# Kernel tuning notes

Hardware: AMD Instinct MI355X
Metric: run time of the kernel (lower is better)

The kernel has to match this reference:

```python
import jax, jax.numpy as jnp
import numpy as np

# Problem dims (match init_kwargs)
N, D, H, W = 32, 64, 56, 56      # Xshape
F, P = 128, 4                    # n_filters, number_of_points
KH = 3                           # h_filter == w_filter
PAD = KH // 2                    # padw
ALPHA = 0.1                      # threshold sharpness for sigmoid approximation


def setup_inputs() -> dict:
    key = jax.random.key(0)
    k1, k2, k3 = jax.random.split(key, 3)
    return {
        "input": jax.random.normal(k1, (N, D, H, W), dtype=jnp.float32),
        # integer kernel coordinates in [0, KH): (filter, point, [ky, kx])
        "kernels": jax.random.randint(k2, (F, P, 2), 0, KH, dtype=jnp.int32),
        # channel projection indices in [0, D): (filter, point)
        "projection_map": jax.random.randint(k3, (F, P), 0, D, dtype=jnp.int32),
    }


def _lbp_forward(x, kernels, projection_map):
    # Pad spatially by PAD (zero padding), as the CUDA kernel pads input.
    xp = jnp.pad(x, ((0, 0), (0, 0), (PAD, PAD), (PAD, PAD)))  # [N, D, H+2P, W+2P]

    # Per (filter, point): gather the HxW window at integer offset (ky, kx)
    # from channel c of the padded input. vmap of dynamic_slice -> one fused gather.
    def sample(c, ky, kx):
        return jax.lax.dynamic_slice(xp, (0, c, ky, kx), (N, 1, H, W))[:, 0]  # [N,H,W]

    samp = jax.vmap(jax.vmap(sample))(
        projection_map, kernels[..., 0], kernels[..., 1]
    )  # [F, P, N, H, W]
    samp = jnp.transpose(samp, (2, 0, 1, 3, 4))  # [N, F, P, H, W]

    # Center pixel (same channel as the sampled point).
    center = xp[:, :, PAD:PAD + H, PAD:PAD + W]       # [N, D, H, W]
    cen = center[:, projection_map]                    # [N, F, P, H, W]

    # Output0: per-point sampled difference; threshold approximated by a
    # steep sigmoid (scale 1/ALPHA) so the op is differentiable, then pool
    # the P bits into a binary code with weights 2^p.
    diff = samp - cen                                  # [N, F, P, H, W]
    bits = jax.nn.sigmoid(diff / ALPHA)
    weights = jnp.asarray(2.0 ** np.arange(P), dtype=jnp.float32)  # [P]
    return jnp.einsum('nfphw,p->nfhw', bits, weights)  # [N, F, H, W]


def reference(input, kernels, projection_map):
    return _lbp_forward(input, kernels, projection_map)
```

## Files before the change

### kernel.cpp

```cpp
#include <hip/hip_runtime.h>


#define NN 32
#define DD 64
#define HH 56
#define WW 56
#define FF 128
#define PP 4

#define ROWS 4
#define TR   (ROWS + 2)
#define TC   64
#define COL0 4
#define CHS  (TR * TC)
#define TILE_DW (DD * CHS)
#define NTHREADS 1024
#define NWAVES 16
#define NPAIR 16
#define NSTRIP (HH / ROWS)
#define FITER (FF / NWAVES)
#define ITEMS (DD * TR * 14)
#define NSLOT 6
#define IMGSTR (DD * HH * WW)

typedef _Float16 h2 __attribute__((ext_vector_type(2)));

static __device__ __forceinline__ uint32_t h2u(h2 h) {
    union { h2 h; uint32_t u; } v; v.h = h; return v.u;
}
static __device__ __forceinline__ h2 u2h(uint32_t u) {
    union { h2 h; uint32_t u; } v; v.u = u; return v.h;
}
static __device__ __forceinline__ h2 splat(float f) {
    h2 r; r.x = (_Float16)f; r.y = (_Float16)f; return r;
}
static __device__ __forceinline__ uint32_t pack2(float a, float b) {
    h2 r; r.x = (_Float16)a; r.y = (_Float16)b; return h2u(r);
}

__global__ __launch_bounds__(NTHREADS, 4) void lbp_kernel(
    const float* __restrict__ x,
    const int*   __restrict__ kern,
    const int*   __restrict__ proj,
    float*       __restrict__ out)
{
    __shared__ uint32_t tile[TILE_DW];

    const int tid = threadIdx.x;
    const int pr  = blockIdx.x;
    const int h0  = blockIdx.y * ROWS;

    const float* x0 = x + (size_t)pr * IMGSTR;
    const float* x1 = x0 + (size_t)NPAIR * IMGSTR;

    float4 av[NSLOT], bv[NSLOT];
    int    lo[NSLOT];
#pragma unroll
    for (int it = 0; it < NSLOT; ++it) {
        const int item = tid + it * NTHREADS;
        av[it] = make_float4(0.f, 0.f, 0.f, 0.f);
        bv[it] = make_float4(0.f, 0.f, 0.f, 0.f);
        lo[it] = -1;
        if (item < ITEMS) {
            const int ch  = item / (TR * 14);
            const int rem = item - ch * (TR * 14);
            const int tr  = rem / 14;
            const int v   = rem - tr * 14;
            lo[it] = ch * CHS + tr * TC + COL0 + 4 * v;
            const int h = h0 + tr - 1;
            if ((unsigned)h < (unsigned)HH) {
                const int off = ch * (HH * WW) + h * WW + 4 * v;
                av[it] = *(const float4*)(x0 + off);
                bv[it] = *(const float4*)(x1 + off);
            }
        }
    }

    if (tid < DD * TR * 2) {
        const int side = tid & 1;
        const int cr   = tid >> 1;
        tile[cr * TC + (side ? 60 : 3)] = 0u;
    }

#pragma unroll
    for (int it = 0; it < NSLOT; ++it) {
        if (lo[it] >= 0) {
            uint4 q;
            q.x = pack2(av[it].x, bv[it].x);
            q.y = pack2(av[it].y, bv[it].y);
            q.z = pack2(av[it].z, bv[it].z);
            q.w = pack2(av[it].w, bv[it].w);
            *(uint4*)(tile + lo[it]) = q;
        }
    }
    __syncthreads();

    const int wid  = __builtin_amdgcn_readfirstlane(tid >> 6);
    const int lane = tid & 63;
    const int w    = lane < WW ? lane : WW - 1;
    const bool act = lane < WW;
    const int cb   = TC + COL0 + w;

    const h2 K0a = splat(2.5f),     K0b = splat(-0.0078f);
    const h2 K1a = splat(1.49146f), K1b = splat(0.08455f);
    const h2 K2a = splat(0.45177f), K2b = splat(0.30774f);
    const h2 KF  = splat(0.49140f);
    const h2 INI = splat(7.5f);

    int f = wid;
    int4 pj = *(const int4*)(proj + f * PP);
    int4 ka = *(const int4*)(kern + f * (PP * 2));
    int4 kb = *(const int4*)(kern + f * (PP * 2) + 4);

#pragma unroll
    for (int k = 0; k < FITER; ++k) {
        const int fn = f + NWAVES;
        int4 pjn = pj, kan = ka, kbn = kb;
        if (k + 1 < FITER) {
            pjn = *(const int4*)(proj + fn * PP);
            kan = *(const int4*)(kern + fn * (PP * 2));
            kbn = *(const int4*)(kern + fn * (PP * 2) + 4);
        }
        const int cc[4]  = {pj.x, pj.y, pj.z, pj.w};
        const int kyv[4] = {ka.x, ka.z, kb.x, kb.z};
        const int kxv[4] = {ka.y, ka.w, kb.y, kb.w};

        uint32_t cu[PP][ROWS], nu[PP][ROWS];
#pragma unroll
        for (int p = 0; p < PP; ++p) {
            const int ky = kyv[p];
            const int kx = kxv[p];
            if (!(ky == 1 && kx == 1)) {
                const int pc = cc[p] * CHS + cb;
                const int pn = pc + (ky - 1) * TC + (kx - 1);
#pragma unroll
                for (int r = 0; r < ROWS; ++r) {
                    cu[p][r] = tile[pc + r * TC];
                    nu[p][r] = tile[pn + r * TC];
                }
            }
        }

        h2 acc[ROWS];
#pragma unroll
        for (int r = 0; r < ROWS; ++r) acc[r] = INI;
#pragma unroll
        for (int p = 0; p < PP; ++p) {
            if (!(kyv[p] == 1 && kxv[p] == 1)) {
                const h2 wt2 = splat((float)(1 << p));
#pragma unroll
                for (int r = 0; r < ROWS; ++r) {
                    const h2 d  = u2h(nu[p][r]) - u2h(cu[p][r]);
                    const uint32_t du = h2u(d);
                    const h2 ad = u2h(du & 0x7FFF7FFFu);
                    const h2 u0 = __builtin_elementwise_fma(K0a, ad, K0b);
                    const h2 u1 = __builtin_elementwise_fma(K1a, ad, K1b);
                    const h2 u2 = __builtin_elementwise_fma(K2a, ad, K2b);
                    const h2 um = __builtin_elementwise_min(
                                      __builtin_elementwise_min(u0, u1),
                                      __builtin_elementwise_min(u2, KF));
                    const uint32_t su = (du & 0x80008000u)
                                      | (h2u(um) & 0x7FFF7FFFu);
                    acc[r] = __builtin_elementwise_fma(wt2, u2h(su), acc[r]);
                }
            }
        }

        if (act) {
            float* o0 = out + ((size_t)pr * FF + f) * (HH * WW)
                            + (size_t)h0 * WW + w;
            float* o1 = o0 + (size_t)NPAIR * FF * (HH * WW);
#pragma unroll
            for (int r = 0; r < ROWS; ++r) {
                o0[r * WW] = (float)acc[r].x;
                o1[r * WW] = (float)acc[r].y;
            }
        }
        f = fn; pj = pjn; ka = kan; kb = kbn;
    }
}

extern "C" void kernel_launch(void* const* d_in, const int* in_sizes, int n_in,
                              void* d_out, int out_size, void* d_ws, size_t ws_size,
                              hipStream_t stream) {
    const float* x    = (const float*)d_in[0];
    const int*   kern = (const int*)d_in[1];
    const int*   proj = (const int*)d_in[2];
    float*       out  = (float*)d_out;

    dim3 grid(NPAIR, NSTRIP);
    dim3 block(NTHREADS);
    lbp_kernel<<<grid, block, 0, stream>>>(x, kern, proj, out);
}
```

Measured before the change: 26.03 us.

## Remap lanes to 4-column groups with vectorized LDS reads and float4 stores

Each wave's 64 lanes now cover 4 rows by 16 groups of 4 columns, where before each lane owned one column across 4 rows. Each lane reads its center and neighbour pixels with 128-bit LDS loads and builds the horizontally shifted neighbours from adjacent uint4 words. Outputs are written as float4 stores. The goal is fewer LDS instructions and wider global stores. The trade-offs are more branching on kx, 8 idle lanes out of 64 instead of 8 out of 64 clamped, and the halo zeroing widened to uint4 stores.

```diff
diff --git a/kernel.cpp b/kernel.cpp
--- a/kernel.cpp
+++ b/kernel.cpp
@@ -79,7 +79,8 @@
     if (tid < DD * TR * 2) {
         const int side = tid & 1;
         const int cr   = tid >> 1;
-        tile[cr * TC + (side ? 60 : 3)] = 0u;
+        *(uint4*)(tile + cr * TC + (side ? 60 : 0)) =
+            make_uint4(0u, 0u, 0u, 0u);
     }
 
 #pragma unroll
@@ -97,9 +98,11 @@
 
     const int wid  = __builtin_amdgcn_readfirstlane(tid >> 6);
     const int lane = tid & 63;
-    const int w    = lane < WW ? lane : WW - 1;
-    const bool act = lane < WW;
-    const int cb   = TC + COL0 + w;
+    const int r    = lane >> 4;
+    const int g    = lane & 15;
+    const bool act = g < 14;
+    const int gc   = act ? g : 13;
+    const int colb = COL0 + 4 * gc;
 
     const h2 K0a = splat(2.5f),     K0b = splat(-0.0078f);
     const h2 K1a = splat(1.49146f), K1b = splat(0.08455f);
@@ -125,56 +128,66 @@
         const int kyv[4] = {ka.x, ka.z, kb.x, kb.z};
         const int kxv[4] = {ka.y, ka.w, kb.y, kb.w};
 
-        uint32_t cu[PP][ROWS], nu[PP][ROWS];
+        h2 acc[4];
+#pragma unroll
+        for (int j = 0; j < 4; ++j) acc[j] = INI;
+
 #pragma unroll
         for (int p = 0; p < PP; ++p) {
             const int ky = kyv[p];
             const int kx = kxv[p];
-            if (!(ky == 1 && kx == 1)) {
-                const int pc = cc[p] * CHS + cb;
-                const int pn = pc + (ky - 1) * TC + (kx - 1);
-#pragma unroll
-                for (int r = 0; r < ROWS; ++r) {
-                    cu[p][r] = tile[pc + r * TC];
-                    nu[p][r] = tile[pn + r * TC];
-                }
+            if (ky == 1 && kx == 1) continue;
+
+            const int cbase = cc[p] * CHS + (1 + r) * TC + colb;
+            const uint4 C = *(const uint4*)(tile + cbase);
+            const int nrow = cc[p] * CHS + (ky + r) * TC;
+
+            uint32_t n0, n1, n2, n3;
+            if (kx == 1) {
+                const uint4 M = *(const uint4*)(tile + nrow + colb);
+                n0 = M.x; n1 = M.y; n2 = M.z; n3 = M.w;
+            } else if (kx == 0) {
+                const uint4 L = *(const uint4*)(tile + nrow + colb - 4);
+                uint4 M;
+                if (ky == 1) M = C;
+                else M = *(const uint4*)(tile + nrow + colb);
+                n0 = L.w; n1 = M.x; n2 = M.y; n3 = M.z;
+            } else {
+                uint4 M;
+                if (ky == 1) M = C;
+                else M = *(const uint4*)(tile + nrow + colb);
+                const uint4 R = *(const uint4*)(tile + nrow + colb + 4);
+                n0 = M.y; n1 = M.z; n2 = M.w; n3 = R.x;
             }
-        }
-
-        h2 acc[ROWS];
-#pragma unroll
-        for (int r = 0; r < ROWS; ++r) acc[r] = INI;
-#pragma unroll
-        for (int p = 0; p < PP; ++p) {
-            if (!(kyv[p] == 1 && kxv[p] == 1)) {
-                const h2 wt2 = splat((float)(1 << p));
-#pragma unroll
-                for (int r = 0; r < ROWS; ++r) {
-                    const h2 d  = u2h(nu[p][r]) - u2h(cu[p][r]);
-                    const uint32_t du = h2u(d);
-                    const h2 ad = u2h(du & 0x7FFF7FFFu);
-                    const h2 u0 = __builtin_elementwise_fma(K0a, ad, K0b);
-                    const h2 u1 = __builtin_elementwise_fma(K1a, ad, K1b);
-                    const h2 u2 = __builtin_elementwise_fma(K2a, ad, K2b);
-                    const h2 um = __builtin_elementwise_min(
-                                      __builtin_elementwise_min(u0, u1),
-                                      __builtin_elementwise_min(u2, KF));
-                    const uint32_t su = (du & 0x80008000u)
-                                      | (h2u(um) & 0x7FFF7FFFu);
-                    acc[r] = __builtin_elementwise_fma(wt2, u2h(su), acc[r]);
-                }
+
+            const uint32_t cu4[4] = {C.x, C.y, C.z, C.w};
+            const uint32_t nu4[4] = {n0, n1, n2, n3};
+            const h2 wt2 = splat((float)(1 << p));
+#pragma unroll
+            for (int j = 0; j < 4; ++j) {
+                const h2 d  = u2h(nu4[j]) - u2h(cu4[j]);
+                const uint32_t du = h2u(d);
+                const h2 ad = u2h(du & 0x7FFF7FFFu);
+                const h2 u0 = __builtin_elementwise_fma(K0a, ad, K0b);
+                const h2 u1 = __builtin_elementwise_fma(K1a, ad, K1b);
+                const h2 u2 = __builtin_elementwise_fma(K2a, ad, K2b);
+                const h2 um = __builtin_elementwise_min(
+                                  __builtin_elementwise_min(u0, u1),
+                                  __builtin_elementwise_min(u2, KF));
+                const uint32_t su = (du & 0x80008000u)
+                                  | (h2u(um) & 0x7FFF7FFFu);
+                acc[j] = __builtin_elementwise_fma(wt2, u2h(su), acc[j]);
             }
         }
 
         if (act) {
             float* o0 = out + ((size_t)pr * FF + f) * (HH * WW)
-                            + (size_t)h0 * WW + w;
+                            + (h0 + r) * WW + 4 * g;
+            *(float4*)o0 = make_float4((float)acc[0].x, (float)acc[1].x,
+                                       (float)acc[2].x, (float)acc[3].x);
             float* o1 = o0 + (size_t)NPAIR * FF * (HH * WW);
-#pragma unroll
-            for (int r = 0; r < ROWS; ++r) {
-                o0[r * WW] = (float)acc[r].x;
-                o1[r * WW] = (float)acc[r].y;
-            }
+            *(float4*)o1 = make_float4((float)acc[0].y, (float)acc[1].y,
+                                       (float)acc[2].y, (float)acc[3].y);
         }
         f = fn; pj = pjn; ka = kan; kb = kbn;
     }
```

Result: slower. 26.98 us (+3.7%).
